# Kernel tuning notes

Measured on AMD Instinct MI355X. Metric: run time of the kernel, lower is better.

Reference implementation:

```python
import jax, jax.numpy as jnp
import numpy as np

B, N, M, C = 8, 8192, 2048, 256
EPS = 1e-8


def setup_inputs() -> dict:
    key = jax.random.key(0)
    k1, k2, k3 = jax.random.split(key, 3)
    unknown = jax.random.uniform(k1, (B, N, 3), dtype=jnp.float32)
    known = jax.random.uniform(k2, (B, M, 3), dtype=jnp.float32)
    known_feats = jax.random.normal(k3, (B, C, M), dtype=jnp.float32)
    return {"unknown": unknown, "known": known, "known_feats": known_feats}


def reference(unknown, known, known_feats):
    # three_nn: brute-force squared distances (B, n, m); pointnet2's CUDA
    # three_nn returns SQUARED distances, matching 1/(d2 + eps) weighting.
    diff = unknown[:, :, None, :] - known[:, None, :, :]  # (B, n, m, 3)
    d2 = jnp.sum(diff * diff, axis=-1)                    # (B, n, m)
    neg_d2, idx = jax.lax.top_k(-d2, 3)                   # 3 smallest distances
    dist = -neg_d2                                        # (B, n, 3)
    dist_recip = 1.0 / (dist + EPS)
    weight = dist_recip / jnp.sum(dist_recip, axis=2, keepdims=True)  # (B, n, 3)
    # three_interpolate: gather the 3 neighbor features and weighted-sum.
    feats_t = jnp.swapaxes(known_feats, 1, 2)             # (B, m, C)
    gathered = jax.vmap(lambda f, i: f[i])(feats_t, idx)  # (B, n, 3, C)
    new_features = jnp.einsum("bnkc,bnk->bcn", gathered, weight)  # (B, C, n)
    return new_features
```

## Files before the change

### kernel.cpp

```cpp
#include <hip/hip_runtime.h>


#define BB 8
#define NN 8192
#define MM 2048
#define CC 256
#define EPSV 1e-8f
#define PTS 128
#define NTH 512
#define NCH 8
#define CHUNK (MM/NCH)
#define TC 4

#define INS(dd, mi, D0,I0,D1,I1,D2,I2) \
    if ((dd) < D2) { \
        if ((dd) < D1) { D2 = D1; I2 = I1; \
            if ((dd) < D0) { D1 = D0; I1 = I0; D0 = (dd); I0 = (mi); } \
            else           { D1 = (dd); I1 = (mi); } \
        } else { D2 = (dd); I2 = (mi); } }

#define PINS(dd, mi, D0,I0,D1,I1,D2,I2) { \
    const bool c0 = (dd) < D0, c1 = (dd) < D1, c2 = (dd) < D2; \
    I2 = c1 ? I1 : (c2 ? (mi) : I2); \
    I1 = c0 ? I0 : (c1 ? (mi) : I1); \
    I0 = c0 ? (mi) : I0; \
    D2 = __builtin_amdgcn_fmed3f(D1, D2, (dd)); \
    D1 = __builtin_amdgcn_fmed3f(D0, D1, (dd)); \
    D0 = fminf(D0, (dd)); }

#define STEP(KX,KY,KZ,MI) { \
    { const float dx = uxA-(KX), dy = uyA-(KY), dz = uzA-(KZ); \
      const float d = __fadd_rn(__fadd_rn(__fmul_rn(dx,dx),__fmul_rn(dy,dy)),__fmul_rn(dz,dz)); \
      PINS(d, MI, dA0,iA0,dA1,iA1,dA2,iA2) } \
    { const float dx = uxB-(KX), dy = uyB-(KY), dz = uzB-(KZ); \
      const float d = __fadd_rn(__fadd_rn(__fmul_rn(dx,dx),__fmul_rn(dy,dy)),__fmul_rn(dz,dz)); \
      PINS(d, MI, dB0,iB0,dB1,iB1,dB2,iB2) } }

__global__ __launch_bounds__(NTH) void nn_scan_kernel(
    const float* __restrict__ unknown,
    const float* __restrict__ known,
    float4* __restrict__ wgt4,
    int4*  __restrict__ idx4)
{
    __shared__ float kxs[MM];
    __shared__ float kys[MM];
    __shared__ float kzs[MM];
    __shared__ float pd[NCH][PTS][3];
    __shared__ int   pi[NCH][PTS][3];

    const int tilesPerBatch = NN / PTS;
    const int b    = blockIdx.x / tilesPerBatch;
    const int tile = blockIdx.x % tilesPerBatch;
    const int t    = threadIdx.x;
    const int p    = t & 63;
    const int g    = t >> 6;

    const float* kb = known + (size_t)b * MM * 3;
    for (int idx = t; idx < MM * 3; idx += NTH) {
        const float v  = kb[idx];
        const int   a  = idx % 3;
        const int   mi = idx / 3;
        float* dst = (a == 0) ? kxs : ((a == 1) ? kys : kzs);
        dst[mi] = v;
    }
    __syncthreads();

    const float* uA = unknown + ((size_t)b * NN + (size_t)tile * PTS + p) * 3;
    const float uxA = uA[0], uyA = uA[1], uzA = uA[2];
    const float* uB = uA + 64 * 3;
    const float uxB = uB[0], uyB = uB[1], uzB = uB[2];

    float dA0=1e30f, dA1=1e30f, dA2=1e30f; int iA0=0, iA1=0, iA2=0;
    float dB0=1e30f, dB1=1e30f, dB2=1e30f; int iB0=0, iB1=0, iB2=0;

    const int mbeg = g * CHUNK;
    #pragma unroll 2
    for (int m = mbeg; m < mbeg + CHUNK; m += 4) {
        const float4 x4 = *reinterpret_cast<const float4*>(&kxs[m]);
        const float4 y4 = *reinterpret_cast<const float4*>(&kys[m]);
        const float4 z4 = *reinterpret_cast<const float4*>(&kzs[m]);
        STEP(x4.x, y4.x, z4.x, m)
        STEP(x4.y, y4.y, z4.y, m+1)
        STEP(x4.z, y4.z, z4.z, m+2)
        STEP(x4.w, y4.w, z4.w, m+3)
    }

    pd[g][p][0] = dA0; pd[g][p][1] = dA1; pd[g][p][2] = dA2;
    pi[g][p][0] = iA0; pi[g][p][1] = iA1; pi[g][p][2] = iA2;
    pd[g][p+64][0] = dB0; pd[g][p+64][1] = dB1; pd[g][p+64][2] = dB2;
    pi[g][p+64][0] = iB0; pi[g][p+64][1] = iB1; pi[g][p+64][2] = iB2;
    __syncthreads();

    if (t < PTS) {
        float e0=1e30f, e1=1e30f, e2=1e30f; int j0=0, j1=0, j2=0;
        #pragma unroll
        for (int q = 0; q < NCH; ++q) {
            #pragma unroll
            for (int r = 0; r < 3; ++r) {
                const float d  = pd[q][t][r];
                const int   ii = pi[q][t][r];
                INS(d, ii, e0,j0,e1,j1,e2,j2)
            }
        }
        const float r0 = 1.0f / (e0 + EPSV);
        const float r1 = 1.0f / (e1 + EPSV);
        const float r2 = 1.0f / (e2 + EPSV);
        const float rs = r0 + r1 + r2;
        const int gp = b * NN + tile * PTS + t;
        wgt4[gp] = make_float4(r0 / rs, r1 / rs, r2 / rs, 0.0f);
        idx4[gp] = make_int4(j0, j1, j2, 0);
    }
}

__global__ __launch_bounds__(NTH) void interp_kernel(
    const float* __restrict__ feats,
    const float4* __restrict__ wgt4,
    const int4*  __restrict__ idx4,
    float* __restrict__ out)
{
    __shared__ float fbuf[TC * MM];

    const int tilesPerB = CC / TC;
    const int b  = blockIdx.x / tilesPerB;
    const int c0 = (blockIdx.x % tilesPerB) * TC;
    const int t  = threadIdx.x;

    const float4* src = reinterpret_cast<const float4*>(
        feats + ((size_t)b * CC + c0) * MM);
    #pragma unroll
    for (int i = t; i < TC * MM / 4; i += NTH)
        reinterpret_cast<float4*>(fbuf)[i] = src[i];
    __syncthreads();

    #pragma unroll 2
    for (int it = 0; it < NN / NTH; ++it) {
        const int n = it * NTH + t;
        const float4 w = wgt4[b * NN + n];
        const int4   j = idx4[b * NN + n];
        float* ob = out + ((size_t)b * CC + c0) * NN + n;
        #pragma unroll
        for (int cl = 0; cl < TC; ++cl) {
            const float* fr = fbuf + cl * MM;
            ob[(size_t)cl * NN] = w.x * fr[j.x] + w.y * fr[j.y] + w.z * fr[j.z];
        }
    }
}

extern "C" void kernel_launch(void* const* d_in, const int* in_sizes, int n_in,
                              void* d_out, int out_size, void* d_ws, size_t ws_size,
                              hipStream_t stream) {
    const float* unknown = (const float*)d_in[0];
    const float* known   = (const float*)d_in[1];
    const float* feats   = (const float*)d_in[2];
    float* out = (float*)d_out;

    float4* wgt4 = (float4*)d_ws;
    int4*   idx4 = (int4*)((char*)d_ws + (size_t)BB * NN * sizeof(float4));

    nn_scan_kernel<<<BB * (NN / PTS), NTH, 0, stream>>>(unknown, known, wgt4, idx4);
    interp_kernel<<<BB * (CC / TC), NTH, 0, stream>>>(feats, wgt4, idx4, out);
}
```

Baseline: 151.8 us.

## Two-pass NN scan with expanded-distance prefilter and exact recheck

```diff
diff --git a/kernel.cpp b/kernel.cpp
--- a/kernel.cpp
+++ b/kernel.cpp
@@ -6,10 +6,12 @@
 #define MM 2048
 #define CC 256
 #define EPSV 1e-8f
-#define PTS 128
 #define NTH 512
 #define NCH 8
 #define CHUNK (MM/NCH)
+#define PPT 4
+#define PTS 256
+#define MARGIN 1e-4f
 #define TC 4
 
 #define INS(dd, mi, D0,I0,D1,I1,D2,I2) \
@@ -19,22 +21,33 @@
             else           { D1 = (dd); I1 = (mi); } \
         } else { D2 = (dd); I2 = (mi); } }
 
-#define PINS(dd, mi, D0,I0,D1,I1,D2,I2) { \
-    const bool c0 = (dd) < D0, c1 = (dd) < D1, c2 = (dd) < D2; \
-    I2 = c1 ? I1 : (c2 ? (mi) : I2); \
-    I1 = c0 ? I0 : (c1 ? (mi) : I1); \
-    I0 = c0 ? (mi) : I0; \
-    D2 = __builtin_amdgcn_fmed3f(D1, D2, (dd)); \
-    D1 = __builtin_amdgcn_fmed3f(D0, D1, (dd)); \
-    D0 = fminf(D0, (dd)); }
-
-#define STEP(KX,KY,KZ,MI) { \
-    { const float dx = uxA-(KX), dy = uyA-(KY), dz = uzA-(KZ); \
-      const float d = __fadd_rn(__fadd_rn(__fmul_rn(dx,dx),__fmul_rn(dy,dy)),__fmul_rn(dz,dz)); \
-      PINS(d, MI, dA0,iA0,dA1,iA1,dA2,iA2) } \
-    { const float dx = uxB-(KX), dy = uyB-(KY), dz = uzB-(KZ); \
-      const float d = __fadd_rn(__fadd_rn(__fmul_rn(dx,dx),__fmul_rn(dy,dy)),__fmul_rn(dz,dz)); \
-      PINS(d, MI, dB0,iB0,dB1,iB1,dB2,iB2) } }
+#define RF(KX,KY,KZ,KQ,J) \
+    __fmaf_rn((KZ), az[J], __fmaf_rn((KY), ay[J], __fmaf_rn((KX), ax[J], (KQ))))
+
+#define S1(KX,KY,KZ,KQ,J) { \
+    const float rr = RF(KX,KY,KZ,KQ,J); \
+    R2[J] = __builtin_amdgcn_fmed3f(R1[J], R2[J], rr); \
+    R1[J] = __builtin_amdgcn_fmed3f(R0[J], R1[J], rr); \
+    R0[J] = fminf(R0[J], rr); }
+
+#define CAP(RR,J,KX,KY,KZ,MI) \
+    if ((RR) <= Tm[J]) { \
+        const float dx = ux[J]-(KX), dy = uy[J]-(KY), dz = uz[J]-(KZ); \
+        const float d = __fadd_rn(__fadd_rn(__fmul_rn(dx,dx),__fmul_rn(dy,dy)),__fmul_rn(dz,dz)); \
+        INS(d, MI, D0[J],J0[J],D1[J],J1[J],D2[J],J2[J]) }
+
+#define S2(KX,KY,KZ,KQ,MI) { \
+    const float rr0 = RF(KX,KY,KZ,KQ,0); \
+    const float rr1 = RF(KX,KY,KZ,KQ,1); \
+    const float rr2 = RF(KX,KY,KZ,KQ,2); \
+    const float rr3 = RF(KX,KY,KZ,KQ,3); \
+    if (fminf(fminf(rr0,rr1),fminf(rr2,rr3)) <= Tmax) { \
+        CAP(rr0,0,KX,KY,KZ,MI) \
+        CAP(rr1,1,KX,KY,KZ,MI) \
+        CAP(rr2,2,KX,KY,KZ,MI) \
+        CAP(rr3,3,KX,KY,KZ,MI) } }
+
+typedef unsigned short u16;
 
 __global__ __launch_bounds__(NTH) void nn_scan_kernel(
     const float* __restrict__ unknown,
@@ -42,17 +55,15 @@
     float4* __restrict__ wgt4,
     int4*  __restrict__ idx4)
 {
-    __shared__ float kxs[MM];
-    __shared__ float kys[MM];
-    __shared__ float kzs[MM];
+    __shared__ float kxs[MM], kys[MM], kzs[MM], kqs[MM];
     __shared__ float pd[NCH][PTS][3];
-    __shared__ int   pi[NCH][PTS][3];
+    __shared__ float Tarr[PTS];
 
     const int tilesPerBatch = NN / PTS;
     const int b    = blockIdx.x / tilesPerBatch;
     const int tile = blockIdx.x % tilesPerBatch;
     const int t    = threadIdx.x;
-    const int p    = t & 63;
+    const int lane = t & 63;
     const int g    = t >> 6;
 
     const float* kb = known + (size_t)b * MM * 3;
@@ -64,41 +75,131 @@
         dst[mi] = v;
     }
     __syncthreads();
-
-    const float* uA = unknown + ((size_t)b * NN + (size_t)tile * PTS + p) * 3;
-    const float uxA = uA[0], uyA = uA[1], uzA = uA[2];
-    const float* uB = uA + 64 * 3;
-    const float uxB = uB[0], uyB = uB[1], uzB = uB[2];
-
-    float dA0=1e30f, dA1=1e30f, dA2=1e30f; int iA0=0, iA1=0, iA2=0;
-    float dB0=1e30f, dB1=1e30f, dB2=1e30f; int iB0=0, iB1=0, iB2=0;
+    for (int m = t; m < MM; m += NTH) {
+        const float x = kxs[m], y = kys[m], z = kzs[m];
+        kqs[m] = __fmaf_rn(z, z, __fmaf_rn(y, y, x * x));
+    }
+
+    const float* ub = unknown + ((size_t)b * NN + (size_t)tile * PTS) * 3;
+    float ux[PPT], uy[PPT], uz[PPT], ax[PPT], ay[PPT], az[PPT];
+    #pragma unroll
+    for (int j = 0; j < PPT; ++j) {
+        const float* u = ub + (size_t)(lane + 64 * j) * 3;
+        ux[j] = u[0]; uy[j] = u[1]; uz[j] = u[2];
+        ax[j] = -2.0f * ux[j]; ay[j] = -2.0f * uy[j]; az[j] = -2.0f * uz[j];
+    }
+    __syncthreads();
+
+    float R0[PPT], R1[PPT], R2[PPT];
+    #pragma unroll
+    for (int j = 0; j < PPT; ++j) { R0[j] = 1e30f; R1[j] = 1e30f; R2[j] = 1e30f; }
 
     const int mbeg = g * CHUNK;
+    #pragma unroll 4
+    for (int m = mbeg; m < mbeg + CHUNK; m += 4) {
+        const float4 x4 = *reinterpret_cast<const float4*>(&kxs[m]);
+        const float4 y4 = *reinterpret_cast<const float4*>(&kys[m]);
+        const float4 z4 = *reinterpret_cast<const float4*>(&kzs[m]);
+        const float4 q4 = *reinterpret_cast<const float4*>(&kqs[m]);
+        #pragma unroll
+        for (int j = 0; j < PPT; ++j) {
+            S1(x4.x, y4.x, z4.x, q4.x, j)
+            S1(x4.y, y4.y, z4.y, q4.y, j)
+            S1(x4.z, y4.z, z4.z, q4.z, j)
+            S1(x4.w, y4.w, z4.w, q4.w, j)
+        }
+    }
+    #pragma unroll
+    for (int j = 0; j < PPT; ++j) {
+        const int p = lane + 64 * j;
+        pd[g][p][0] = R0[j]; pd[g][p][1] = R1[j]; pd[g][p][2] = R2[j];
+    }
+    __syncthreads();
+
+    if (t < PTS) {
+        float e0 = 1e30f, e1 = 1e30f, e2 = 1e30f;
+        #pragma unroll
+        for (int q = 0; q < NCH; ++q) {
+            #pragma unroll
+            for (int r = 0; r < 3; ++r) {
+                const float d = pd[q][t][r];
+                e2 = __builtin_amdgcn_fmed3f(e1, e2, d);
+                e1 = __builtin_amdgcn_fmed3f(e0, e1, d);
+                e0 = fminf(e0, d);
+            }
+        }
+        Tarr[t] = e2 + MARGIN;
+    }
+    __syncthreads();
+
+    float D0[PPT], D1[PPT], D2[PPT];
+    int   J0[PPT], J1[PPT], J2[PPT];
+    float Tm[PPT];
+    #pragma unroll
+    for (int j = 0; j < PPT; ++j) {
+        D0[j] = 1e30f; D1[j] = 1e30f; D2[j] = 1e30f;
+        J0[j] = 0; J1[j] = 0; J2[j] = 0;
+        Tm[j] = Tarr[lane + 64 * j];
+    }
+    const float Tmax = fmaxf(fmaxf(Tm[0], Tm[1]), fmaxf(Tm[2], Tm[3]));
+
     #pragma unroll 2
     for (int m = mbeg; m < mbeg + CHUNK; m += 4) {
         const float4 x4 = *reinterpret_cast<const float4*>(&kxs[m]);
         const float4 y4 = *reinterpret_cast<const float4*>(&kys[m]);
         const float4 z4 = *reinterpret_cast<const float4*>(&kzs[m]);
-        STEP(x4.x, y4.x, z4.x, m)
-        STEP(x4.y, y4.y, z4.y, m+1)
-        STEP(x4.z, y4.z, z4.z, m+2)
-        STEP(x4.w, y4.w, z4.w, m+3)
-    }
-
-    pd[g][p][0] = dA0; pd[g][p][1] = dA1; pd[g][p][2] = dA2;
-    pi[g][p][0] = iA0; pi[g][p][1] = iA1; pi[g][p][2] = iA2;
-    pd[g][p+64][0] = dB0; pd[g][p+64][1] = dB1; pd[g][p+64][2] = dB2;
-    pi[g][p+64][0] = iB0; pi[g][p+64][1] = iB1; pi[g][p+64][2] = iB2;
-    __syncthreads();
-
+        const float4 q4 = *reinterpret_cast<const float4*>(&kqs[m]);
+        S2(x4.x, y4.x, z4.x, q4.x, m)
+        S2(x4.y, y4.y, z4.y, q4.y, m+1)
+        S2(x4.z, y4.z, z4.z, q4.z, m+2)
+        S2(x4.w, y4.w, z4.w, q4.w, m+3)
+    }
+
+    float (*sd)[PTS][3] = pd;
+    u16 (*si)[PTS][3] = reinterpret_cast<u16 (*)[PTS][3]>(&pd[4][0][0]);
+
+    if (g < 4) {
+        #pragma unroll
+        for (int j = 0; j < PPT; ++j) {
+            const int p = lane + 64 * j;
+            sd[g][p][0] = D0[j]; sd[g][p][1] = D1[j]; sd[g][p][2] = D2[j];
+            si[g][p][0] = (u16)J0[j]; si[g][p][1] = (u16)J1[j]; si[g][p][2] = (u16)J2[j];
+        }
+    }
+    __syncthreads();
+
+    float e0 = 1e30f, e1 = 1e30f, e2 = 1e30f;
+    int   j0 = 0,     j1 = 0,     j2 = 0;
     if (t < PTS) {
-        float e0=1e30f, e1=1e30f, e2=1e30f; int j0=0, j1=0, j2=0;
-        #pragma unroll
-        for (int q = 0; q < NCH; ++q) {
+        #pragma unroll
+        for (int q = 0; q < 4; ++q) {
             #pragma unroll
             for (int r = 0; r < 3; ++r) {
-                const float d  = pd[q][t][r];
-                const int   ii = pi[q][t][r];
+                const float d  = sd[q][t][r];
+                const int   ii = (int)si[q][t][r];
+                INS(d, ii, e0,j0,e1,j1,e2,j2)
+            }
+        }
+    }
+    __syncthreads();
+
+    if (g >= 4) {
+        #pragma unroll
+        for (int j = 0; j < PPT; ++j) {
+            const int p = lane + 64 * j;
+            sd[g-4][p][0] = D0[j]; sd[g-4][p][1] = D1[j]; sd[g-4][p][2] = D2[j];
+            si[g-4][p][0] = (u16)J0[j]; si[g-4][p][1] = (u16)J1[j]; si[g-4][p][2] = (u16)J2[j];
+        }
+    }
+    __syncthreads();
+
+    if (t < PTS) {
+        #pragma unroll
+        for (int q = 0; q < 4; ++q) {
+            #pragma unroll
+            for (int r = 0; r < 3; ++r) {
+                const float d  = sd[q][t][r];
+                const int   ii = (int)si[q][t][r];
                 INS(d, ii, e0,j0,e1,j1,e2,j2)
             }
         }
```

Result: slower. 169.6 us (+11.7%).

## Two-pass NN scan using expanded-distance filter then exact candidate refinement

Applied to the files above, without the earlier changes.

```diff
diff --git a/kernel.cpp b/kernel.cpp
--- a/kernel.cpp
+++ b/kernel.cpp
@@ -6,10 +6,11 @@
 #define MM 2048
 #define CC 256
 #define EPSV 1e-8f
-#define PTS 128
 #define NTH 512
 #define NCH 8
 #define CHUNK (MM/NCH)
+#define PTS 64
+#define MARGIN 1e-4f
 #define TC 4
 
 #define INS(dd, mi, D0,I0,D1,I1,D2,I2) \
@@ -19,22 +20,22 @@
             else           { D1 = (dd); I1 = (mi); } \
         } else { D2 = (dd); I2 = (mi); } }
 
-#define PINS(dd, mi, D0,I0,D1,I1,D2,I2) { \
-    const bool c0 = (dd) < D0, c1 = (dd) < D1, c2 = (dd) < D2; \
-    I2 = c1 ? I1 : (c2 ? (mi) : I2); \
-    I1 = c0 ? I0 : (c1 ? (mi) : I1); \
-    I0 = c0 ? (mi) : I0; \
-    D2 = __builtin_amdgcn_fmed3f(D1, D2, (dd)); \
-    D1 = __builtin_amdgcn_fmed3f(D0, D1, (dd)); \
-    D0 = fminf(D0, (dd)); }
-
-#define STEP(KX,KY,KZ,MI) { \
-    { const float dx = uxA-(KX), dy = uyA-(KY), dz = uzA-(KZ); \
-      const float d = __fadd_rn(__fadd_rn(__fmul_rn(dx,dx),__fmul_rn(dy,dy)),__fmul_rn(dz,dz)); \
-      PINS(d, MI, dA0,iA0,dA1,iA1,dA2,iA2) } \
-    { const float dx = uxB-(KX), dy = uyB-(KY), dz = uzB-(KZ); \
-      const float d = __fadd_rn(__fadd_rn(__fmul_rn(dx,dx),__fmul_rn(dy,dy)),__fmul_rn(dz,dz)); \
-      PINS(d, MI, dB0,iB0,dB1,iB1,dB2,iB2) } }
+#define RF(KX,KY,KZ,KQ) \
+    __fmaf_rn((KZ), az, __fmaf_rn((KY), ay, __fmaf_rn((KX), ax, (KQ))))
+
+#define S1(KX,KY,KZ,KQ) { \
+    const float rr = RF(KX,KY,KZ,KQ); \
+    R2 = __builtin_amdgcn_fmed3f(R1, R2, rr); \
+    R1 = __builtin_amdgcn_fmed3f(R0, R1, rr); \
+    R0 = fminf(R0, rr); }
+
+#define CAP(RR,KX,KY,KZ,MI) \
+    if ((RR) <= Tm) { \
+        const float dx = ux-(KX), dy = uy-(KY), dz = uz-(KZ); \
+        const float d = __fadd_rn(__fadd_rn(__fmul_rn(dx,dx),__fmul_rn(dy,dy)),__fmul_rn(dz,dz)); \
+        INS(d, MI, D0,J0,D1,J1,D2,J2) }
+
+typedef unsigned short u16;
 
 __global__ __launch_bounds__(NTH) void nn_scan_kernel(
     const float* __restrict__ unknown,
@@ -42,17 +43,16 @@
     float4* __restrict__ wgt4,
     int4*  __restrict__ idx4)
 {
-    __shared__ float kxs[MM];
-    __shared__ float kys[MM];
-    __shared__ float kzs[MM];
+    __shared__ float kxs[MM], kys[MM], kzs[MM], kqs[MM];
     __shared__ float pd[NCH][PTS][3];
-    __shared__ int   pi[NCH][PTS][3];
+    __shared__ u16   si[NCH][PTS][3];
+    __shared__ float Tarr[PTS];
 
     const int tilesPerBatch = NN / PTS;
     const int b    = blockIdx.x / tilesPerBatch;
     const int tile = blockIdx.x % tilesPerBatch;
     const int t    = threadIdx.x;
-    const int p    = t & 63;
+    const int lane = t & 63;
     const int g    = t >> 6;
 
     const float* kb = known + (size_t)b * MM * 3;
@@ -64,41 +64,83 @@
         dst[mi] = v;
     }
     __syncthreads();
-
-    const float* uA = unknown + ((size_t)b * NN + (size_t)tile * PTS + p) * 3;
-    const float uxA = uA[0], uyA = uA[1], uzA = uA[2];
-    const float* uB = uA + 64 * 3;
-    const float uxB = uB[0], uyB = uB[1], uzB = uB[2];
-
-    float dA0=1e30f, dA1=1e30f, dA2=1e30f; int iA0=0, iA1=0, iA2=0;
-    float dB0=1e30f, dB1=1e30f, dB2=1e30f; int iB0=0, iB1=0, iB2=0;
-
+    for (int m = t; m < MM; m += NTH) {
+        const float x = kxs[m], y = kys[m], z = kzs[m];
+        kqs[m] = __fmaf_rn(z, z, __fmaf_rn(y, y, x * x));
+    }
+
+    const float* u = unknown + ((size_t)b * NN + (size_t)tile * PTS + lane) * 3;
+    const float ux = u[0], uy = u[1], uz = u[2];
+    const float ax = -2.0f * ux, ay = -2.0f * uy, az = -2.0f * uz;
+    __syncthreads();
+
+    float R0 = 1e30f, R1 = 1e30f, R2 = 1e30f;
     const int mbeg = g * CHUNK;
+    #pragma unroll 4
+    for (int m = mbeg; m < mbeg + CHUNK; m += 4) {
+        const float4 x4 = *reinterpret_cast<const float4*>(&kxs[m]);
+        const float4 y4 = *reinterpret_cast<const float4*>(&kys[m]);
+        const float4 z4 = *reinterpret_cast<const float4*>(&kzs[m]);
+        const float4 q4 = *reinterpret_cast<const float4*>(&kqs[m]);
+        S1(x4.x, y4.x, z4.x, q4.x)
+        S1(x4.y, y4.y, z4.y, q4.y)
+        S1(x4.z, y4.z, z4.z, q4.z)
+        S1(x4.w, y4.w, z4.w, q4.w)
+    }
+    pd[g][lane][0] = R0; pd[g][lane][1] = R1; pd[g][lane][2] = R2;
+    __syncthreads();
+
+    if (t < PTS) {
+        float e0 = 1e30f, e1 = 1e30f, e2 = 1e30f;
+        #pragma unroll
+        for (int q = 0; q < NCH; ++q) {
+            #pragma unroll
+            for (int r = 0; r < 3; ++r) {
+                const float d = pd[q][t][r];
+                e2 = __builtin_amdgcn_fmed3f(e1, e2, d);
+                e1 = __builtin_amdgcn_fmed3f(e0, e1, d);
+                e0 = fminf(e0, d);
+            }
+        }
+        Tarr[t] = e2 + MARGIN;
+    }
+    __syncthreads();
+
+    float D0 = 1e30f, D1 = 1e30f, D2 = 1e30f;
+    int   J0 = 0,     J1 = 0,     J2 = 0;
+    const float Tm = Tarr[lane];
+
     #pragma unroll 2
     for (int m = mbeg; m < mbeg + CHUNK; m += 4) {
         const float4 x4 = *reinterpret_cast<const float4*>(&kxs[m]);
         const float4 y4 = *reinterpret_cast<const float4*>(&kys[m]);
         const float4 z4 = *reinterpret_cast<const float4*>(&kzs[m]);
-        STEP(x4.x, y4.x, z4.x, m)
-        STEP(x4.y, y4.y, z4.y, m+1)
-        STEP(x4.z, y4.z, z4.z, m+2)
-        STEP(x4.w, y4.w, z4.w, m+3)
-    }
-
-    pd[g][p][0] = dA0; pd[g][p][1] = dA1; pd[g][p][2] = dA2;
-    pi[g][p][0] = iA0; pi[g][p][1] = iA1; pi[g][p][2] = iA2;
-    pd[g][p+64][0] = dB0; pd[g][p+64][1] = dB1; pd[g][p+64][2] = dB2;
-    pi[g][p+64][0] = iB0; pi[g][p+64][1] = iB1; pi[g][p+64][2] = iB2;
+        const float4 q4 = *reinterpret_cast<const float4*>(&kqs[m]);
+        const float rr0 = RF(x4.x, y4.x, z4.x, q4.x);
+        const float rr1 = RF(x4.y, y4.y, z4.y, q4.y);
+        const float rr2 = RF(x4.z, y4.z, z4.z, q4.z);
+        const float rr3 = RF(x4.w, y4.w, z4.w, q4.w);
+        if (fminf(fminf(rr0, rr1), fminf(rr2, rr3)) <= Tm) {
+            CAP(rr0, x4.x, y4.x, z4.x, m)
+            CAP(rr1, x4.y, y4.y, z4.y, m+1)
+            CAP(rr2, x4.z, y4.z, z4.z, m+2)
+            CAP(rr3, x4.w, y4.w, z4.w, m+3)
+        }
+    }
+
+    pd[g][lane][0] = D0; pd[g][lane][1] = D1; pd[g][lane][2] = D2;
+    si[g][lane][0] = (u16)J0; si[g][lane][1] = (u16)J1; si[g][lane][2] = (u16)J2;
     __syncthreads();
 
     if (t < PTS) {
-        float e0=1e30f, e1=1e30f, e2=1e30f; int j0=0, j1=0, j2=0;
+        float e0 = 1e30f, e1 = 1e30f, e2 = 1e30f;
+        int   j0 = 0,     j1 = 0,     j2 = 0;
         #pragma unroll
         for (int q = 0; q < NCH; ++q) {
             #pragma unroll
             for (int r = 0; r < 3; ++r) {
                 const float d  = pd[q][t][r];
-                const int   ii = pi[q][t][r];
+                const int   ii = (int)si[q][t][r];
                 INS(d, ii, e0,j0,e1,j1,e2,j2)
             }
         }
```

Result: faster. 147.4 us (-2.9%).
